# Kernel optimization log

Measured on AMD Instinct MI355X. Metric: run time of the kernel, lower is better.

Reference implementation:

```python
import jax, jax.numpy as jnp
import numpy as np

N, E, D, H, O = 100000, 1600000, 128, 64, 64


def setup_inputs() -> dict:
    key = jax.random.key(0)
    ks = jax.random.split(key, 6)
    src = jax.random.randint(ks[0], (E,), 0, N)
    dst = jax.random.randint(ks[1], (E,), 0, N)
    emb = jax.random.normal(ks[2], (N, D), jnp.float32) * 0.02  # embedding table
    W1 = jax.random.normal(ks[3], (D, H), jnp.float32) / np.sqrt(D)
    b1 = jnp.zeros((H,), jnp.float32)
    W2 = jax.random.normal(ks[4], (H, O), jnp.float32) / np.sqrt(H)
    b2 = jnp.zeros((O,), jnp.float32)
    return dict(emb=emb, W1=W1, b1=b1, W2=W2, b2=b2, src=src, dst=dst)


def gcn_conv(x, W, b, src, dst):
    # PyG GCNConv: add self-loops, symmetric deg^{-1/2} norm, linear -> gather -> scatter-add, bias
    n = x.shape[0]
    loop = jnp.arange(n, dtype=src.dtype)
    s = jnp.concatenate([src, loop])
    d = jnp.concatenate([dst, loop])
    x = x @ W  # [n, out]
    deg = jax.ops.segment_sum(jnp.ones_like(d, dtype=x.dtype), d, num_segments=n)
    dinv = jnp.where(deg > 0, jax.lax.rsqrt(deg), 0.0)
    norm = dinv[s] * dinv[d]  # [E+n]
    out = jax.ops.segment_sum(x[s] * norm[:, None], d, num_segments=n)
    return out + b


def reference(emb, W1, b1, W2, b2, src, dst):
    # node_ids = unique(edge_index) == arange(N) for contiguous ids -> lookup is whole table
    x = emb
    x = jax.nn.relu(gcn_conv(x, W1, b1, src, dst))
    return gcn_conv(x, W2, b2, src, dst)
```

## Files before the change

kernel.cpp:

```cpp
#include <hip/hip_runtime.h>

constexpr int FD = 64;
constexpr int P  = 8;
constexpr int WN = 125;
constexpr int SRC_BITS = 17;
constexpr int SRC_MASK = (1 << SRC_BITS) - 1;
constexpr int G1S = 16;

typedef __attribute__((ext_vector_type(8))) short bf16x8;
typedef __attribute__((ext_vector_type(4))) float f32x4;

__device__ __forceinline__ int part_of(int d, unsigned long long M) {
    return (int)(((unsigned long long)(unsigned)d * M) >> 32);
}
__device__ __forceinline__ unsigned short bf16r(float x) {
    unsigned u = __float_as_uint(x);
    return (unsigned short)((u + 0x7FFFu + ((u >> 16) & 1u)) >> 16);
}
__device__ __forceinline__ unsigned bf16pack(float a, float b) {
    unsigned ua = __float_as_uint(a), ub = __float_as_uint(b);
    ua = (ua + 0x7FFFu + ((ua >> 16) & 1u)) >> 16;
    ub = (ub + 0x7FFFu + ((ub >> 16) & 1u)) >> 16;
    return ua | (ub << 16);
}
__device__ __forceinline__ float4 bf16x4u(uint2 u) {
    float4 v;
    v.x = __uint_as_float(u.x << 16);
    v.y = __uint_as_float(u.x & 0xFFFF0000u);
    v.z = __uint_as_float(u.y << 16);
    v.w = __uint_as_float(u.y & 0xFFFF0000u);
    return v;
}

__global__ void k_pre(int* __restrict__ gcur1, int cap1,
                      int* __restrict__ gcur2, int cap2, int NW,
                      const float* __restrict__ W1, const float* __restrict__ W2,
                      unsigned short* __restrict__ Wt1, unsigned short* __restrict__ Wt2) {
    int i = blockIdx.x * 256 + threadIdx.x;
    if (i < P)  gcur1[i * G1S] = i * cap1;
    if (i < NW) gcur2[i] = i * cap2;
    if (i < 64 * 128) {
        int c = i >> 7, k = i & 127;
        Wt1[i] = bf16r(W1[(size_t)k * 64 + c]);
    }
    int j = i - 64 * 128;
    if (j >= 0 && j < 64 * 64) {
        int c = j >> 6, k = j & 63;
        Wt2[j] = bf16r(W2[(size_t)k * 64 + c]);
    }
}

__global__ __launch_bounds__(256) void k_part8(const int* __restrict__ src,
                                               const int* __restrict__ dst, int E,
                                               unsigned long long M, int npp,
                                               int* __restrict__ gcur1, int cap1,
                                               int* __restrict__ p1) {
    constexpr int CH = 1024;
    __shared__ int hh[P], bbase[P], lcur[P];
    if (threadIdx.x < P) hh[threadIdx.x] = 0;
    __syncthreads();
    const int e0  = blockIdx.x * CH;
    const int rem = min(CH, E - e0);
    const int lane = threadIdx.x & 63;
    const unsigned long long lmlt = (lane == 63) ? ~0ull >> 1 : (1ull << lane) - 1;

    int dv[4], sv[4], bv[4], ldr[4], rnk[4], cnt[4];
    bool val[4];
#pragma unroll
    for (int j = 0; j < 4; ++j) {
        int i = j * 256 + threadIdx.x;
        val[j] = i < rem;
        int e = e0 + (val[j] ? i : 0);
        dv[j] = __builtin_nontemporal_load(&dst[e]);
        sv[j] = __builtin_nontemporal_load(&src[e]);
        bv[j] = part_of(dv[j], M);
    }
#pragma unroll
    for (int j = 0; j < 4; ++j) {
        unsigned long long m0 = __ballot(val[j] && (bv[j] & 1));
        unsigned long long m1 = __ballot(val[j] && (bv[j] & 2));
        unsigned long long m2 = __ballot(val[j] && (bv[j] & 4));
        unsigned long long mv = __ballot(val[j]);
        unsigned long long t = ((bv[j] & 1) ? m0 : ~m0)
                             & ((bv[j] & 2) ? m1 : ~m1)
                             & ((bv[j] & 4) ? m2 : ~m2) & mv;
        ldr[j] = __ffsll((unsigned long long)t) - 1;
        rnk[j] = __popcll(t & lmlt);
        cnt[j] = __popcll(t);
        if (val[j] && lane == ldr[j]) atomicAdd(&hh[bv[j]], cnt[j]);
    }
    __syncthreads();
    if (threadIdx.x < P) {
        bbase[threadIdx.x] = atomicAdd(&gcur1[threadIdx.x * G1S], hh[threadIdx.x]);
        lcur[threadIdx.x] = 0;
    }
    __syncthreads();
#pragma unroll
    for (int j = 0; j < 4; ++j) {
        int wb = 0;
        if (val[j] && lane == ldr[j]) wb = atomicAdd(&lcur[bv[j]], cnt[j]);
        wb = __shfl(wb, ldr[j] < 0 ? 0 : ldr[j], 64);
        if (val[j]) {
            int pos = bbase[bv[j]] + wb + rnk[j];
            if (pos < (bv[j] + 1) * cap1)
                p1[pos] = ((dv[j] - bv[j] * npp) << SRC_BITS) | sv[j];
        }
    }
}

__global__ __launch_bounds__(256) void k_partwin(const int* __restrict__ p1,
                                                 const int* __restrict__ gcur1, int cap1,
                                                 int npp, unsigned long long M2,
                                                 int* __restrict__ gcur2, int cap2,
                                                 int* __restrict__ p2) {
    constexpr int CH = 1024;
    constexpr int MAXW = 128;
    __shared__ int hh[MAXW], wbase[MAXW], lcur[MAXW];
    const int p   = blockIdx.x & (P - 1);
    const int j   = blockIdx.x >> 3;
    const int wlo = (p * npp) / WN;
    const int whi = ((p + 1) * npp - 1) / WN;
    const int nw  = whi - wlo + 1;
    const int lo = p * cap1 + j * CH;
    const int hi = min(lo + CH, gcur1[p * G1S]);
    if (lo >= hi) return;
    for (int t = threadIdx.x; t < nw; t += 256) hh[t] = 0;
    __syncthreads();
    int pk[4], wv[4];
    bool val[4];
#pragma unroll
    for (int q = 0; q < 4; ++q) {
        int e = lo + q * 256 + threadIdx.x;
        val[q] = e < hi;
        pk[q] = val[q] ? __builtin_nontemporal_load(&p1[e]) : 0;
        int d = p * npp + (pk[q] >> SRC_BITS);
        wv[q] = (int)(((unsigned long long)(unsigned)d * M2) >> 32);
        if (val[q]) atomicAdd(&hh[wv[q] - wlo], 1);
    }
    __syncthreads();
    for (int t = threadIdx.x; t < nw; t += 256) {
        wbase[t] = hh[t] ? atomicAdd(&gcur2[wlo + t], hh[t]) : 0;
        lcur[t] = 0;
    }
    __syncthreads();
#pragma unroll
    for (int q = 0; q < 4; ++q) {
        if (val[q]) {
            int w  = wv[q];
            int hw = w - wlo;
            int d  = p * npp + (pk[q] >> SRC_BITS);
            int pos = wbase[hw] + atomicAdd(&lcur[hw], 1);
            if (pos < (w + 1) * cap2)
                p2[pos] = ((d - w * WN) << SRC_BITS) | (pk[q] & SRC_MASK);
        }
    }
}

__global__ __launch_bounds__(256) void k_sortwin(int* __restrict__ p2,
                                                 const int* __restrict__ gcur2, int cap2,
                                                 int* __restrict__ rowinfo,
                                                 float* __restrict__ dinv, int N) {
    __shared__ int hist[WN], beg[WN], cur[WN];
    const int w  = blockIdx.x;
    const int lo = w * cap2;
    const int hi = min(gcur2[w], lo + cap2);
    const int cnt = hi - lo;
    for (int t = threadIdx.x; t < WN; t += 256) hist[t] = 0;
    __syncthreads();
    int pk[10];
#pragma unroll
    for (int j = 0; j < 10; ++j) {
        int i = j * 256 + threadIdx.x;
        pk[j] = (i < cnt) ? p2[lo + i] : -1;
        if (pk[j] >= 0) atomicAdd(&hist[pk[j] >> SRC_BITS], 1);
    }
    __syncthreads();
    if (threadIdx.x < 64) {
        int lane = threadIdx.x;
        int v0 = hist[lane];
        int x0 = v0;
#pragma unroll
        for (int o = 1; o < 64; o <<= 1) { int y = __shfl_up(x0, o, 64); if (lane >= o) x0 += y; }
        int tot0 = __shfl(x0, 63, 64);
        int v1 = (lane < WN - 64) ? hist[64 + lane] : 0;
        int x1 = v1;
#pragma unroll
        for (int o = 1; o < 64; o <<= 1) { int y = __shfl_up(x1, o, 64); if (lane >= o) x1 += y; }
        int b0 = x0 - v0;
        beg[lane] = b0; cur[lane] = b0;
        if (lane < WN - 64) {
            int b1 = tot0 + x1 - v1;
            beg[64 + lane] = b1; cur[64 + lane] = b1;
        }
    }
    __syncthreads();
#pragma unroll
    for (int j = 0; j < 10; ++j) {
        if (pk[j] >= 0) {
            int ld  = pk[j] >> SRC_BITS;
            int pos = atomicAdd(&cur[ld], 1);
            p2[lo + pos] = pk[j] & SRC_MASK;
        }
    }
    for (int t = threadIdx.x; t < WN; t += 256) {
        int node = w * WN + t;
        if (node < N) {
            rowinfo[node] = beg[t] | (hist[t] << 16);
            dinv[node] = rsqrtf((float)(hist[t] + 1));
        }
    }
}

__global__ __launch_bounds__(256) void k_gemm1(const float* __restrict__ Xf,
                                               const uint4* __restrict__ Wt,
                                               const float* __restrict__ dinv,
                                               unsigned short* __restrict__ Yb,
                                               int n) {
    constexpr int K = 128, NT = 4, RQ4 = 16;
    const int wv = threadIdx.x >> 6;
    const int l  = threadIdx.x & 63;
    const int r  = l & 15, hi = l >> 4;
    const int row = blockIdx.x * 64 + wv * 16 + r;
    union U { uint4 u; bf16x8 v; };
    f32x4 acc[4] = {};

#pragma unroll
    for (int t = 0; t < NT; ++t) {
        U a;
        float4 f0 = make_float4(0.f, 0.f, 0.f, 0.f);
        float4 f1 = make_float4(0.f, 0.f, 0.f, 0.f);
        if (row < n) {
            f0 = *(const float4*)&Xf[(size_t)row * K + t * 32 + hi * 8];
            f1 = *(const float4*)&Xf[(size_t)row * K + t * 32 + hi * 8 + 4];
        }
        a.u.x = bf16pack(f0.x, f0.y);
        a.u.y = bf16pack(f0.z, f0.w);
        a.u.z = bf16pack(f1.x, f1.y);
        a.u.w = bf16pack(f1.z, f1.w);
#pragma unroll
        for (int cb = 0; cb < 4; ++cb) {
            U b;
            b.u = Wt[(size_t)(cb * 16 + r) * RQ4 + t * 4 + hi];
            acc[cb] = __builtin_amdgcn_mfma_f32_16x16x32_bf16(a.v, b.v, acc[cb], 0, 0, 0);
        }
    }
    const int orow0 = blockIdx.x * 64 + wv * 16 + hi * 4;
#pragma unroll
    for (int j = 0; j < 4; ++j) {
        int orow = orow0 + j;
        if (orow < n) {
            float sc = dinv[orow];
#pragma unroll
            for (int cb = 0; cb < 4; ++cb)
                Yb[(size_t)orow * 64 + cb * 16 + r] = bf16r(acc[cb][j] * sc);
        }
    }
}

__global__ __launch_bounds__(256) void k_agg_fuse(const unsigned* __restrict__ Xb,
                                                  const int* __restrict__ col,
                                                  const int* __restrict__ rowinfo, int cap2,
                                                  const float* __restrict__ dinv,
                                                  const float* __restrict__ bias,
                                                  const uint4* __restrict__ Wt2,
                                                  unsigned short* __restrict__ Yb,
                                                  int n) {
    __shared__ __align__(16) unsigned hrow[16][36];
    const int node0 = blockIdx.x * 16;
    {
        int t = blockIdx.x * 256 + threadIdx.x;
        int node = t >> 4;
        int lane = t & 15;
        int nl   = threadIdx.x >> 4;
        float ox = 0.f, oy = 0.f, oz = 0.f, ow = 0.f;
        if (node < n) {
            int info = rowinfo[node];
            int w    = (int)((unsigned)node / WN);
            int beg  = w * cap2 + (info & 0xFFFF);
            int end  = beg + (info >> 16);
            const uint2* Xv = (const uint2*)Xb;
            uint2 svu = Xv[(size_t)node * 16 + lane];
            float4 a0 = {0,0,0,0}, a1 = {0,0,0,0}, a2 = {0,0,0,0}, a3 = {0,0,0,0};
            int e = beg;
            for (; e + 8 <= end; e += 8) {
                int s0 = col[e],     s1 = col[e + 1], s2 = col[e + 2], s3 = col[e + 3];
                int s4 = col[e + 4], s5 = col[e + 5], s6 = col[e + 6], s7 = col[e + 7];
                uint2 u0 = Xv[(size_t)s0 * 16 + lane];
                uint2 u1 = Xv[(size_t)s1 * 16 + lane];
                uint2 u2 = Xv[(size_t)s2 * 16 + lane];
                uint2 u3 = Xv[(size_t)s3 * 16 + lane];
                uint2 u4 = Xv[(size_t)s4 * 16 + lane];
                uint2 u5 = Xv[(size_t)s5 * 16 + lane];
                uint2 u6 = Xv[(size_t)s6 * 16 + lane];
                uint2 u7 = Xv[(size_t)s7 * 16 + lane];
                float4 v0 = bf16x4u(u0), v1 = bf16x4u(u1), v2 = bf16x4u(u2), v3 = bf16x4u(u3);
                float4 v4 = bf16x4u(u4), v5 = bf16x4u(u5), v6 = bf16x4u(u6), v7 = bf16x4u(u7);
                a0.x += v0.x; a0.y += v0.y; a0.z += v0.z; a0.w += v0.w;
                a1.x += v1.x; a1.y += v1.y; a1.z += v1.z; a1.w += v1.w;
                a2.x += v2.x; a2.y += v2.y; a2.z += v2.z; a2.w += v2.w;
                a3.x += v3.x; a3.y += v3.y; a3.z += v3.z; a3.w += v3.w;
                a0.x += v4.x; a0.y += v4.y; a0.z += v4.z; a0.w += v4.w;
                a1.x += v5.x; a1.y += v5.y; a1.z += v5.z; a1.w += v5.w;
                a2.x += v6.x; a2.y += v6.y; a2.z += v6.z; a2.w += v6.w;
                a3.x += v7.x; a3.y += v7.y; a3.z += v7.z; a3.w += v7.w;
            }
            for (; e + 4 <= end; e += 4) {
                int s0 = col[e], s1 = col[e + 1], s2 = col[e + 2], s3 = col[e + 3];
                uint2 u0 = Xv[(size_t)s0 * 16 + lane];
                uint2 u1 = Xv[(size_t)s1 * 16 + lane];
                uint2 u2 = Xv[(size_t)s2 * 16 + lane];
                uint2 u3 = Xv[(size_t)s3 * 16 + lane];
                float4 v0 = bf16x4u(u0), v1 = bf16x4u(u1), v2 = bf16x4u(u2), v3 = bf16x4u(u3);
                a0.x += v0.x; a0.y += v0.y; a0.z += v0.z; a0.w += v0.w;
                a1.x += v1.x; a1.y += v1.y; a1.z += v1.z; a1.w += v1.w;
                a2.x += v2.x; a2.y += v2.y; a2.z += v2.z; a2.w += v2.w;
                a3.x += v3.x; a3.y += v3.y; a3.z += v3.z; a3.w += v3.w;
            }
            for (; e < end; ++e) {
                float4 v = bf16x4u(Xv[(size_t)col[e] * 16 + lane]);
                a0.x += v.x; a0.y += v.y; a0.z += v.z; a0.w += v.w;
            }
            float4 sv = bf16x4u(svu);
            float sx = a0.x + a1.x + a2.x + a3.x + sv.x;
            float sy = a0.y + a1.y + a2.y + a3.y + sv.y;
            float sz = a0.z + a1.z + a2.z + a3.z + sv.z;
            float sw = a0.w + a1.w + a2.w + a3.w + sv.w;
            float di = dinv[node];
            float4 b = ((const float4*)bias)[lane];
            ox = fmaxf(fmaf(di, sx, b.x), 0.f);
            oy = fmaxf(fmaf(di, sy, b.y), 0.f);
            oz = fmaxf(fmaf(di, sz, b.z), 0.f);
            ow = fmaxf(fmaf(di, sw, b.w), 0.f);
        }
        hrow[nl][lane * 2]     = bf16pack(ox, oy);
        hrow[nl][lane * 2 + 1] = bf16pack(oz, ow);
    }
    __syncthreads();
    {
        const int wv = threadIdx.x >> 6;
        const int l  = threadIdx.x & 63;
        const int r  = l & 15, hi = l >> 4;
        union U { uint4 u; bf16x8 v; };
        f32x4 acc = {};
#pragma unroll
        for (int t = 0; t < 2; ++t) {
            U a, b;
            a.u = *(const uint4*)&hrow[r][t * 16 + hi * 4];
            b.u = Wt2[(size_t)(wv * 16 + r) * 8 + t * 4 + hi];
            acc = __builtin_amdgcn_mfma_f32_16x16x32_bf16(a.v, b.v, acc, 0, 0, 0);
        }
#pragma unroll
        for (int j = 0; j < 4; ++j) {
            int node = node0 + hi * 4 + j;
            if (node < n)
                Yb[(size_t)node * 64 + wv * 16 + r] = bf16r(acc[j] * dinv[node]);
        }
    }
}

__global__ __launch_bounds__(256) void k_agg_f32(const unsigned* __restrict__ Xb,
                                                 const int* __restrict__ col,
                                                 const int* __restrict__ rowinfo, int cap2,
                                                 const float* __restrict__ dinv,
                                                 const float* __restrict__ bias,
                                                 float* __restrict__ out, int n) {
    int t = blockIdx.x * 256 + threadIdx.x;
    int node = t >> 4;
    int lane = t & 15;
    if (node >= n) return;
    int info = rowinfo[node];
    int w    = (int)((unsigned)node / WN);
    int beg  = w * cap2 + (info & 0xFFFF);
    int end  = beg + (info >> 16);
    const uint2* Xv = (const uint2*)Xb;
    uint2 svu = Xv[(size_t)node * 16 + lane];
    float4 a0 = {0,0,0,0}, a1 = {0,0,0,0}, a2 = {0,0,0,0}, a3 = {0,0,0,0};
    int e = beg;
    for (; e + 8 <= end; e += 8) {
        int s0 = col[e],     s1 = col[e + 1], s2 = col[e + 2], s3 = col[e + 3];
        int s4 = col[e + 4], s5 = col[e + 5], s6 = col[e + 6], s7 = col[e + 7];
        uint2 u0 = Xv[(size_t)s0 * 16 + lane];
        uint2 u1 = Xv[(size_t)s1 * 16 + lane];
        uint2 u2 = Xv[(size_t)s2 * 16 + lane];
        uint2 u3 = Xv[(size_t)s3 * 16 + lane];
        uint2 u4 = Xv[(size_t)s4 * 16 + lane];
        uint2 u5 = Xv[(size_t)s5 * 16 + lane];
        uint2 u6 = Xv[(size_t)s6 * 16 + lane];
        uint2 u7 = Xv[(size_t)s7 * 16 + lane];
        float4 v0 = bf16x4u(u0), v1 = bf16x4u(u1), v2 = bf16x4u(u2), v3 = bf16x4u(u3);
        float4 v4 = bf16x4u(u4), v5 = bf16x4u(u5), v6 = bf16x4u(u6), v7 = bf16x4u(u7);
        a0.x += v0.x; a0.y += v0.y; a0.z += v0.z; a0.w += v0.w;
        a1.x += v1.x; a1.y += v1.y; a1.z += v1.z; a1.w += v1.w;
        a2.x += v2.x; a2.y += v2.y; a2.z += v2.z; a2.w += v2.w;
        a3.x += v3.x; a3.y += v3.y; a3.z += v3.z; a3.w += v3.w;
        a0.x += v4.x; a0.y += v4.y; a0.z += v4.z; a0.w += v4.w;
        a1.x += v5.x; a1.y += v5.y; a1.z += v5.z; a1.w += v5.w;
        a2.x += v6.x; a2.y += v6.y; a2.z += v6.z; a2.w += v6.w;
        a3.x += v7.x; a3.y += v7.y; a3.z += v7.z; a3.w += v7.w;
    }
    for (; e + 4 <= end; e += 4) {
        int s0 = col[e], s1 = col[e + 1], s2 = col[e + 2], s3 = col[e + 3];
        uint2 u0 = Xv[(size_t)s0 * 16 + lane];
        uint2 u1 = Xv[(size_t)s1 * 16 + lane];
        uint2 u2 = Xv[(size_t)s2 * 16 + lane];
        uint2 u3 = Xv[(size_t)s3 * 16 + lane];
        float4 v0 = bf16x4u(u0), v1 = bf16x4u(u1), v2 = bf16x4u(u2), v3 = bf16x4u(u3);
        a0.x += v0.x; a0.y += v0.y; a0.z += v0.z; a0.w += v0.w;
        a1.x += v1.x; a1.y += v1.y; a1.z += v1.z; a1.w += v1.w;
        a2.x += v2.x; a2.y += v2.y; a2.z += v2.z; a2.w += v2.w;
        a3.x += v3.x; a3.y += v3.y; a3.z += v3.z; a3.w += v3.w;
    }
    for (; e < end; ++e) {
        float4 v = bf16x4u(Xv[(size_t)col[e] * 16 + lane]);
        a0.x += v.x; a0.y += v.y; a0.z += v.z; a0.w += v.w;
    }
    float4 sv = bf16x4u(svu);
    float sx = a0.x + a1.x + a2.x + a3.x + sv.x;
    float sy = a0.y + a1.y + a2.y + a3.y + sv.y;
    float sz = a0.z + a1.z + a2.z + a3.z + sv.z;
    float sw = a0.w + a1.w + a2.w + a3.w + sv.w;
    float di = dinv[node];
    float4 b = ((const float4*)bias)[lane];
    float4 o;
    o.x = fmaf(di, sx, b.x);
    o.y = fmaf(di, sy, b.y);
    o.z = fmaf(di, sz, b.z);
    o.w = fmaf(di, sw, b.w);
    ((float4*)(out + (size_t)node * FD))[lane] = o;
}


extern "C" void kernel_launch(void* const* d_in, const int* in_sizes, int n_in,
                              void* d_out, int out_size, void* d_ws, size_t ws_size,
                              hipStream_t stream) {
    const float* emb = (const float*)d_in[0];
    const float* W1  = (const float*)d_in[1];
    const float* b1  = (const float*)d_in[2];
    const float* W2  = (const float*)d_in[3];
    const float* b2  = (const float*)d_in[4];
    const int*   src = (const int*)d_in[5];
    const int*   dst = (const int*)d_in[6];

    const int D = 128;
    const int N = in_sizes[0] / D;
    const int E = in_sizes[5];
    float* out = (float*)d_out;

    const int npp  = (N + P - 1) / P;
    const int NW   = (N + WN - 1) / WN;
    const int cap1 = E / P + 16384;
    int cap2 = E / NW + 560;
    if (cap2 > 2560) cap2 = 2560;

    const unsigned long long M  = ((1ull << 32) + npp - 1) / npp;
    const unsigned long long M2 = ((1ull << 32) + WN - 1) / WN;

    unsigned* Ab1  = (unsigned*)d_ws;
    unsigned* Ab2  = Ab1 + (size_t)N * 32;
    int*   p2      = (int*)(Ab2 + (size_t)N * 32);
    int*   rowinfo = p2 + (size_t)NW * cap2;
    float* dinv    = (float*)(rowinfo + N);
    int*   gcur1   = (int*)(dinv + N);
    int*   gcur2   = gcur1 + P * G1S;
    unsigned short* Wt1 = (unsigned short*)(gcur2 + ((NW + 3) & ~3));
    unsigned short* Wt2 = Wt1 + 64 * 128;
    int*   p1      = (int*)Ab1;

    k_pre<<<48, 256, 0, stream>>>(gcur1, cap1, gcur2, cap2, NW, W1, W2, Wt1, Wt2);
    k_part8<<<(E + 1023) / 1024, 256, 0, stream>>>(src, dst, E, M, npp, gcur1, cap1, p1);
    int nb2 = (cap1 + 1023) / 1024;
    k_partwin<<<P * nb2, 256, 0, stream>>>(p1, gcur1, cap1, npp, M2, gcur2, cap2, p2);
    k_sortwin<<<NW, 256, 0, stream>>>(p2, gcur2, cap2, rowinfo, dinv, N);

    k_gemm1<<<(N + 63) / 64, 256, 0, stream>>>(emb, (const uint4*)Wt1, dinv, (unsigned short*)Ab1, N);
    k_agg_fuse<<<(N + 15) / 16, 256, 0, stream>>>(Ab1, p2, rowinfo, cap2, dinv, b1,
                                                  (const uint4*)Wt2, (unsigned short*)Ab2, N);
    k_agg_f32<<<(N * 16 + 255) / 256, 256, 0, stream>>>(Ab2, p2, rowinfo, cap2, dinv, b2, out, N);
}
```

Baseline: 171.7 us.

## Degree-sort nodes within windows and use 8-lane uint4 gathers in aggregation

The window sort now also counting-sorts the nodes of each window by in-degree and writes a permuted rowinfo plus a node-id map. Both aggregation kernels walk these degree-sorted slots, so neighbouring 8-lane groups in a wavefront have similar loop trip counts and less divergence. Each node now uses 8 lanes loading 16-byte uint4 rows instead of 16 lanes loading 8-byte rows, and the fused kernel handles 32 nodes per block with two MFMAs per wave. The cost is an extra indirection through nid, scattered output writes, less unrolling, and extra shared-memory scan work in the sort kernel.

```diff
diff --git a/kernel.cpp b/kernel.cpp
--- a/kernel.cpp
+++ b/kernel.cpp
@@ -23,13 +23,11 @@
     ub = (ub + 0x7FFFu + ((ub >> 16) & 1u)) >> 16;
     return ua | (ub << 16);
 }
-__device__ __forceinline__ float4 bf16x4u(uint2 u) {
-    float4 v;
-    v.x = __uint_as_float(u.x << 16);
-    v.y = __uint_as_float(u.x & 0xFFFF0000u);
-    v.z = __uint_as_float(u.y << 16);
-    v.w = __uint_as_float(u.y & 0xFFFF0000u);
-    return v;
+__device__ __forceinline__ void addu4(float4& A, float4& B, uint4 u) {
+    A.x += __uint_as_float(u.x << 16); A.y += __uint_as_float(u.x & 0xFFFF0000u);
+    A.z += __uint_as_float(u.y << 16); A.w += __uint_as_float(u.y & 0xFFFF0000u);
+    B.x += __uint_as_float(u.z << 16); B.y += __uint_as_float(u.z & 0xFFFF0000u);
+    B.z += __uint_as_float(u.w << 16); B.w += __uint_as_float(u.w & 0xFFFF0000u);
 }
 
 __global__ void k_pre(int* __restrict__ gcur1, int cap1,
@@ -158,14 +156,16 @@
 
 __global__ __launch_bounds__(256) void k_sortwin(int* __restrict__ p2,
                                                  const int* __restrict__ gcur2, int cap2,
-                                                 int* __restrict__ rowinfo,
+                                                 int* __restrict__ rowinfo2,
+                                                 int* __restrict__ nid,
                                                  float* __restrict__ dinv, int N) {
-    __shared__ int hist[WN], beg[WN], cur[WN];
+    __shared__ int hist[WN], beg[WN], cur[WN], dh[64], dbs[64];
     const int w  = blockIdx.x;
     const int lo = w * cap2;
     const int hi = min(gcur2[w], lo + cap2);
     const int cnt = hi - lo;
     for (int t = threadIdx.x; t < WN; t += 256) hist[t] = 0;
+    if (threadIdx.x < 64) dh[threadIdx.x] = 0;
     __syncthreads();
     int pk[10];
 #pragma unroll
@@ -193,6 +193,11 @@
             beg[64 + lane] = b1; cur[64 + lane] = b1;
         }
     }
+    int mybin = -1, myir = 0;
+    if (threadIdx.x < WN) {
+        mybin = min(hist[threadIdx.x], 63);
+        myir  = atomicAdd(&dh[mybin], 1);
+    }
     __syncthreads();
 #pragma unroll
     for (int j = 0; j < 10; ++j) {
@@ -202,10 +207,22 @@
             p2[lo + pos] = pk[j] & SRC_MASK;
         }
     }
-    for (int t = threadIdx.x; t < WN; t += 256) {
+    if (threadIdx.x < 64) {
+        int lane = threadIdx.x;
+        int v = dh[lane], x = v;
+#pragma unroll
+        for (int o = 1; o < 64; o <<= 1) { int y = __shfl_up(x, o, 64); if (lane >= o) x += y; }
+        dbs[lane] = x - v;
+    }
+    __syncthreads();
+    if (threadIdx.x < WN) {
+        int t = threadIdx.x;
         int node = w * WN + t;
         if (node < N) {
-            rowinfo[node] = beg[t] | (hist[t] << 16);
+            int rank = dbs[mybin] + myir;
+            int slot = w * WN + rank;
+            rowinfo2[slot] = beg[t] | (hist[t] << 16);
+            nid[slot] = node;
             dinv[node] = rsqrtf((float)(hist[t] + 1));
         }
     }
@@ -257,176 +274,138 @@
     }
 }
 
-__global__ __launch_bounds__(256) void k_agg_fuse(const unsigned* __restrict__ Xb,
+__global__ __launch_bounds__(256) void k_agg_fuse(const uint4* __restrict__ Xr,
                                                   const int* __restrict__ col,
-                                                  const int* __restrict__ rowinfo, int cap2,
+                                                  const int* __restrict__ rowinfo2,
+                                                  const int* __restrict__ nid,
+                                                  int cap2, unsigned long long M2,
                                                   const float* __restrict__ dinv,
                                                   const float* __restrict__ bias,
                                                   const uint4* __restrict__ Wt2,
                                                   unsigned short* __restrict__ Yb,
                                                   int n) {
-    __shared__ __align__(16) unsigned hrow[16][36];
-    const int node0 = blockIdx.x * 16;
+    __shared__ __align__(16) unsigned hrow[32][36];
+    __shared__ int nidB[32];
     {
-        int t = blockIdx.x * 256 + threadIdx.x;
-        int node = t >> 4;
-        int lane = t & 15;
-        int nl   = threadIdx.x >> 4;
-        float ox = 0.f, oy = 0.f, oz = 0.f, ow = 0.f;
-        if (node < n) {
-            int info = rowinfo[node];
-            int w    = (int)((unsigned)node / WN);
+        int slot = blockIdx.x * 32 + (threadIdx.x >> 3);
+        int lane = threadIdx.x & 7;
+        int sb   = threadIdx.x >> 3;
+        float4 h0 = {0,0,0,0}, h1 = {0,0,0,0};
+        int node = -1;
+        if (slot < n) {
+            int info = rowinfo2[slot];
+            node     = nid[slot];
+            int w    = (int)(((unsigned long long)(unsigned)slot * M2) >> 32);
             int beg  = w * cap2 + (info & 0xFFFF);
             int end  = beg + (info >> 16);
-            const uint2* Xv = (const uint2*)Xb;
-            uint2 svu = Xv[(size_t)node * 16 + lane];
-            float4 a0 = {0,0,0,0}, a1 = {0,0,0,0}, a2 = {0,0,0,0}, a3 = {0,0,0,0};
+            uint4 svu = Xr[(size_t)node * 8 + lane];
+            float4 p0 = {0,0,0,0}, p1 = {0,0,0,0}, q0 = {0,0,0,0}, q1 = {0,0,0,0};
             int e = beg;
-            for (; e + 8 <= end; e += 8) {
-                int s0 = col[e],     s1 = col[e + 1], s2 = col[e + 2], s3 = col[e + 3];
-                int s4 = col[e + 4], s5 = col[e + 5], s6 = col[e + 6], s7 = col[e + 7];
-                uint2 u0 = Xv[(size_t)s0 * 16 + lane];
-                uint2 u1 = Xv[(size_t)s1 * 16 + lane];
-                uint2 u2 = Xv[(size_t)s2 * 16 + lane];
-                uint2 u3 = Xv[(size_t)s3 * 16 + lane];
-                uint2 u4 = Xv[(size_t)s4 * 16 + lane];
-                uint2 u5 = Xv[(size_t)s5 * 16 + lane];
-                uint2 u6 = Xv[(size_t)s6 * 16 + lane];
-                uint2 u7 = Xv[(size_t)s7 * 16 + lane];
-                float4 v0 = bf16x4u(u0), v1 = bf16x4u(u1), v2 = bf16x4u(u2), v3 = bf16x4u(u3);
-                float4 v4 = bf16x4u(u4), v5 = bf16x4u(u5), v6 = bf16x4u(u6), v7 = bf16x4u(u7);
-                a0.x += v0.x; a0.y += v0.y; a0.z += v0.z; a0.w += v0.w;
-                a1.x += v1.x; a1.y += v1.y; a1.z += v1.z; a1.w += v1.w;
-                a2.x += v2.x; a2.y += v2.y; a2.z += v2.z; a2.w += v2.w;
-                a3.x += v3.x; a3.y += v3.y; a3.z += v3.z; a3.w += v3.w;
-                a0.x += v4.x; a0.y += v4.y; a0.z += v4.z; a0.w += v4.w;
-                a1.x += v5.x; a1.y += v5.y; a1.z += v5.z; a1.w += v5.w;
-                a2.x += v6.x; a2.y += v6.y; a2.z += v6.z; a2.w += v6.w;
-                a3.x += v7.x; a3.y += v7.y; a3.z += v7.z; a3.w += v7.w;
-            }
             for (; e + 4 <= end; e += 4) {
                 int s0 = col[e], s1 = col[e + 1], s2 = col[e + 2], s3 = col[e + 3];
-                uint2 u0 = Xv[(size_t)s0 * 16 + lane];
-                uint2 u1 = Xv[(size_t)s1 * 16 + lane];
-                uint2 u2 = Xv[(size_t)s2 * 16 + lane];
-                uint2 u3 = Xv[(size_t)s3 * 16 + lane];
-                float4 v0 = bf16x4u(u0), v1 = bf16x4u(u1), v2 = bf16x4u(u2), v3 = bf16x4u(u3);
-                a0.x += v0.x; a0.y += v0.y; a0.z += v0.z; a0.w += v0.w;
-                a1.x += v1.x; a1.y += v1.y; a1.z += v1.z; a1.w += v1.w;
-                a2.x += v2.x; a2.y += v2.y; a2.z += v2.z; a2.w += v2.w;
-                a3.x += v3.x; a3.y += v3.y; a3.z += v3.z; a3.w += v3.w;
+                uint4 u0 = Xr[(size_t)s0 * 8 + lane];
+                uint4 u1 = Xr[(size_t)s1 * 8 + lane];
+                uint4 u2 = Xr[(size_t)s2 * 8 + lane];
+                uint4 u3 = Xr[(size_t)s3 * 8 + lane];
+                addu4(p0, p1, u0); addu4(q0, q1, u1);
+                addu4(p0, p1, u2); addu4(q0, q1, u3);
             }
-            for (; e < end; ++e) {
-                float4 v = bf16x4u(Xv[(size_t)col[e] * 16 + lane]);
-                a0.x += v.x; a0.y += v.y; a0.z += v.z; a0.w += v.w;
-            }
-            float4 sv = bf16x4u(svu);
-            float sx = a0.x + a1.x + a2.x + a3.x + sv.x;
-            float sy = a0.y + a1.y + a2.y + a3.y + sv.y;
-            float sz = a0.z + a1.z + a2.z + a3.z + sv.z;
-            float sw = a0.w + a1.w + a2.w + a3.w + sv.w;
+            for (; e < end; ++e)
+                addu4(p0, p1, Xr[(size_t)col[e] * 8 + lane]);
+            addu4(p0, p1, svu);
             float di = dinv[node];
-            float4 b = ((const float4*)bias)[lane];
-            ox = fmaxf(fmaf(di, sx, b.x), 0.f);
-            oy = fmaxf(fmaf(di, sy, b.y), 0.f);
-            oz = fmaxf(fmaf(di, sz, b.z), 0.f);
-            ow = fmaxf(fmaf(di, sw, b.w), 0.f);
-        }
-        hrow[nl][lane * 2]     = bf16pack(ox, oy);
-        hrow[nl][lane * 2 + 1] = bf16pack(oz, ow);
+            float4 b0 = ((const float4*)bias)[lane * 2];
+            float4 b1 = ((const float4*)bias)[lane * 2 + 1];
+            h0.x = fmaxf(fmaf(di, p0.x + q0.x, b0.x), 0.f);
+            h0.y = fmaxf(fmaf(di, p0.y + q0.y, b0.y), 0.f);
+            h0.z = fmaxf(fmaf(di, p0.z + q0.z, b0.z), 0.f);
+            h0.w = fmaxf(fmaf(di, p0.w + q0.w, b0.w), 0.f);
+            h1.x = fmaxf(fmaf(di, p1.x + q1.x, b1.x), 0.f);
+            h1.y = fmaxf(fmaf(di, p1.y + q1.y, b1.y), 0.f);
+            h1.z = fmaxf(fmaf(di, p1.z + q1.z, b1.z), 0.f);
+            h1.w = fmaxf(fmaf(di, p1.w + q1.w, b1.w), 0.f);
+        }
+        hrow[sb][lane * 4 + 0] = bf16pack(h0.x, h0.y);
+        hrow[sb][lane * 4 + 1] = bf16pack(h0.z, h0.w);
+        hrow[sb][lane * 4 + 2] = bf16pack(h1.x, h1.y);
+        hrow[sb][lane * 4 + 3] = bf16pack(h1.z, h1.w);
+        if (lane == 0) nidB[sb] = node;
     }
     __syncthreads();
     {
         const int wv = threadIdx.x >> 6;
         const int l  = threadIdx.x & 63;
         const int r  = l & 15, hi = l >> 4;
+        const int rt = wv >> 1, cb0 = (wv & 1) * 2;
         union U { uint4 u; bf16x8 v; };
-        f32x4 acc = {};
+        f32x4 acc0 = {}, acc1 = {};
 #pragma unroll
         for (int t = 0; t < 2; ++t) {
-            U a, b;
-            a.u = *(const uint4*)&hrow[r][t * 16 + hi * 4];
-            b.u = Wt2[(size_t)(wv * 16 + r) * 8 + t * 4 + hi];
-            acc = __builtin_amdgcn_mfma_f32_16x16x32_bf16(a.v, b.v, acc, 0, 0, 0);
+            U a, b0, b1;
+            a.u  = *(const uint4*)&hrow[rt * 16 + r][t * 16 + hi * 4];
+            b0.u = Wt2[(size_t)((cb0 + 0) * 16 + r) * 8 + t * 4 + hi];
+            b1.u = Wt2[(size_t)((cb0 + 1) * 16 + r) * 8 + t * 4 + hi];
+            acc0 = __builtin_amdgcn_mfma_f32_16x16x32_bf16(a.v, b0.v, acc0, 0, 0, 0);
+            acc1 = __builtin_amdgcn_mfma_f32_16x16x32_bf16(a.v, b1.v, acc1, 0, 0, 0);
         }
 #pragma unroll
         for (int j = 0; j < 4; ++j) {
-            int node = node0 + hi * 4 + j;
-            if (node < n)
-                Yb[(size_t)node * 64 + wv * 16 + r] = bf16r(acc[j] * dinv[node]);
-        }
-    }
-}
-
-__global__ __launch_bounds__(256) void k_agg_f32(const unsigned* __restrict__ Xb,
+            int node = nidB[rt * 16 + hi * 4 + j];
+            if (node >= 0) {
+                float sc = dinv[node];
+                Yb[(size_t)node * 64 + (cb0 + 0) * 16 + r] = bf16r(acc0[j] * sc);
+                Yb[(size_t)node * 64 + (cb0 + 1) * 16 + r] = bf16r(acc1[j] * sc);
+            }
+        }
+    }
+}
+
+__global__ __launch_bounds__(256) void k_agg_f32(const uint4* __restrict__ Xr,
                                                  const int* __restrict__ col,
-                                                 const int* __restrict__ rowinfo, int cap2,
+                                                 const int* __restrict__ rowinfo2,
+                                                 const int* __restrict__ nid,
+                                                 int cap2, unsigned long long M2,
                                                  const float* __restrict__ dinv,
                                                  const float* __restrict__ bias,
                                                  float* __restrict__ out, int n) {
-    int t = blockIdx.x * 256 + threadIdx.x;
-    int node = t >> 4;
-    int lane = t & 15;
-    if (node >= n) return;
-    int info = rowinfo[node];
-    int w    = (int)((unsigned)node / WN);
+    int slot = blockIdx.x * 32 + (threadIdx.x >> 3);
+    int lane = threadIdx.x & 7;
+    if (slot >= n) return;
+    int info = rowinfo2[slot];
+    int node = nid[slot];
+    int w    = (int)(((unsigned long long)(unsigned)slot * M2) >> 32);
     int beg  = w * cap2 + (info & 0xFFFF);
     int end  = beg + (info >> 16);
-    const uint2* Xv = (const uint2*)Xb;
-    uint2 svu = Xv[(size_t)node * 16 + lane];
-    float4 a0 = {0,0,0,0}, a1 = {0,0,0,0}, a2 = {0,0,0,0}, a3 = {0,0,0,0};
+    uint4 svu = Xr[(size_t)node * 8 + lane];
+    float4 p0 = {0,0,0,0}, p1 = {0,0,0,0}, q0 = {0,0,0,0}, q1 = {0,0,0,0};
     int e = beg;
-    for (; e + 8 <= end; e += 8) {
-        int s0 = col[e],     s1 = col[e + 1], s2 = col[e + 2], s3 = col[e + 3];
-        int s4 = col[e + 4], s5 = col[e + 5], s6 = col[e + 6], s7 = col[e + 7];
-        uint2 u0 = Xv[(size_t)s0 * 16 + lane];
-        uint2 u1 = Xv[(size_t)s1 * 16 + lane];
-        uint2 u2 = Xv[(size_t)s2 * 16 + lane];
-        uint2 u3 = Xv[(size_t)s3 * 16 + lane];
-        uint2 u4 = Xv[(size_t)s4 * 16 + lane];
-        uint2 u5 = Xv[(size_t)s5 * 16 + lane];
-        uint2 u6 = Xv[(size_t)s6 * 16 + lane];
-        uint2 u7 = Xv[(size_t)s7 * 16 + lane];
-        float4 v0 = bf16x4u(u0), v1 = bf16x4u(u1), v2 = bf16x4u(u2), v3 = bf16x4u(u3);
-        float4 v4 = bf16x4u(u4), v5 = bf16x4u(u5), v6 = bf16x4u(u6), v7 = bf16x4u(u7);
-        a0.x += v0.x; a0.y += v0.y; a0.z += v0.z; a0.w += v0.w;
-        a1.x += v1.x; a1.y += v1.y; a1.z += v1.z; a1.w += v1.w;
-        a2.x += v2.x; a2.y += v2.y; a2.z += v2.z; a2.w += v2.w;
-        a3.x += v3.x; a3.y += v3.y; a3.z += v3.z; a3.w += v3.w;
-        a0.x += v4.x; a0.y += v4.y; a0.z += v4.z; a0.w += v4.w;
-        a1.x += v5.x; a1.y += v5.y; a1.z += v5.z; a1.w += v5.w;
-        a2.x += v6.x; a2.y += v6.y; a2.z += v6.z; a2.w += v6.w;
-        a3.x += v7.x; a3.y += v7.y; a3.z += v7.z; a3.w += v7.w;
-    }
     for (; e + 4 <= end; e += 4) {
         int s0 = col[e], s1 = col[e + 1], s2 = col[e + 2], s3 = col[e + 3];
-        uint2 u0 = Xv[(size_t)s0 * 16 + lane];
-        uint2 u1 = Xv[(size_t)s1 * 16 + lane];
-        uint2 u2 = Xv[(size_t)s2 * 16 + lane];
-        uint2 u3 = Xv[(size_t)s3 * 16 + lane];
-        float4 v0 = bf16x4u(u0), v1 = bf16x4u(u1), v2 = bf16x4u(u2), v3 = bf16x4u(u3);
-        a0.x += v0.x; a0.y += v0.y; a0.z += v0.z; a0.w += v0.w;
-        a1.x += v1.x; a1.y += v1.y; a1.z += v1.z; a1.w += v1.w;
-        a2.x += v2.x; a2.y += v2.y; a2.z += v2.z; a2.w += v2.w;
-        a3.x += v3.x; a3.y += v3.y; a3.z += v3.z; a3.w += v3.w;
-    }
-    for (; e < end; ++e) {
-        float4 v = bf16x4u(Xv[(size_t)col[e] * 16 + lane]);
-        a0.x += v.x; a0.y += v.y; a0.z += v.z; a0.w += v.w;
-    }
-    float4 sv = bf16x4u(svu);
-    float sx = a0.x + a1.x + a2.x + a3.x + sv.x;
-    float sy = a0.y + a1.y + a2.y + a3.y + sv.y;
-    float sz = a0.z + a1.z + a2.z + a3.z + sv.z;
-    float sw = a0.w + a1.w + a2.w + a3.w + sv.w;
+        uint4 u0 = Xr[(size_t)s0 * 8 + lane];
+        uint4 u1 = Xr[(size_t)s1 * 8 + lane];
+        uint4 u2 = Xr[(size_t)s2 * 8 + lane];
+        uint4 u3 = Xr[(size_t)s3 * 8 + lane];
+        addu4(p0, p1, u0); addu4(q0, q1, u1);
+        addu4(p0, p1, u2); addu4(q0, q1, u3);
+    }
+    for (; e < end; ++e)
+        addu4(p0, p1, Xr[(size_t)col[e] * 8 + lane]);
+    addu4(p0, p1, svu);
     float di = dinv[node];
-    float4 b = ((const float4*)bias)[lane];
-    float4 o;
-    o.x = fmaf(di, sx, b.x);
-    o.y = fmaf(di, sy, b.y);
-    o.z = fmaf(di, sz, b.z);
-    o.w = fmaf(di, sw, b.w);
-    ((float4*)(out + (size_t)node * FD))[lane] = o;
+    float4 b0 = ((const float4*)bias)[lane * 2];
+    float4 b1 = ((const float4*)bias)[lane * 2 + 1];
+    float4 o0, o1;
+    o0.x = fmaf(di, p0.x + q0.x, b0.x);
+    o0.y = fmaf(di, p0.y + q0.y, b0.y);
+    o0.z = fmaf(di, p0.z + q0.z, b0.z);
+    o0.w = fmaf(di, p0.w + q0.w, b0.w);
+    o1.x = fmaf(di, p1.x + q1.x, b1.x);
+    o1.y = fmaf(di, p1.y + q1.y, b1.y);
+    o1.z = fmaf(di, p1.z + q1.z, b1.z);
+    o1.w = fmaf(di, p1.w + q1.w, b1.w);
+    float4* orow = (float4*)(out + (size_t)node * FD);
+    orow[lane * 2]     = o0;
+    orow[lane * 2 + 1] = o1;
 }
 
 
@@ -458,8 +437,9 @@
     unsigned* Ab1  = (unsigned*)d_ws;
     unsigned* Ab2  = Ab1 + (size_t)N * 32;
     int*   p2      = (int*)(Ab2 + (size_t)N * 32);
-    int*   rowinfo = p2 + (size_t)NW * cap2;
-    float* dinv    = (float*)(rowinfo + N);
+    int*   rowinfo2= p2 + (size_t)NW * cap2;
+    int*   nid     = rowinfo2 + N;
+    float* dinv    = (float*)(nid + N);
     int*   gcur1   = (int*)(dinv + N);
     int*   gcur2   = gcur1 + P * G1S;
     unsigned short* Wt1 = (unsigned short*)(gcur2 + ((NW + 3) & ~3));
@@ -470,10 +450,12 @@
     k_part8<<<(E + 1023) / 1024, 256, 0, stream>>>(src, dst, E, M, npp, gcur1, cap1, p1);
     int nb2 = (cap1 + 1023) / 1024;
     k_partwin<<<P * nb2, 256, 0, stream>>>(p1, gcur1, cap1, npp, M2, gcur2, cap2, p2);
-    k_sortwin<<<NW, 256, 0, stream>>>(p2, gcur2, cap2, rowinfo, dinv, N);
+    k_sortwin<<<NW, 256, 0, stream>>>(p2, gcur2, cap2, rowinfo2, nid, dinv, N);
 
     k_gemm1<<<(N + 63) / 64, 256, 0, stream>>>(emb, (const uint4*)Wt1, dinv, (unsigned short*)Ab1, N);
-    k_agg_fuse<<<(N + 15) / 16, 256, 0, stream>>>(Ab1, p2, rowinfo, cap2, dinv, b1,
-                                                  (const uint4*)Wt2, (unsigned short*)Ab2, N);
-    k_agg_f32<<<(N * 16 + 255) / 256, 256, 0, stream>>>(Ab2, p2, rowinfo, cap2, dinv, b2, out, N);
-}
+    k_agg_fuse<<<(N * 8 + 255) / 256, 256, 0, stream>>>((const uint4*)Ab1, p2, rowinfo2, nid,
+                                                        cap2, M2, dinv, b1,
+                                                        (const uint4*)Wt2, (unsigned short*)Ab2, N);
+    k_agg_f32<<<(N * 8 + 255) / 256, 256, 0, stream>>>((const uint4*)Ab2, p2, rowinfo2, nid,
+                                                       cap2, M2, dinv, b2, out, N);
+}
```

Result: no change. 171.2 us (median of 2 runs) (-0.3%).
